# Kernel optimization log

Measured on AMD Instinct MI355X. Metric: run time of the kernel, lower is better.

Reference implementation:

```python
import jax, jax.numpy as jnp
import numpy as np

D_MODEL = 1024
D_INNER = 2048
D_STATE = 16
D_CONV = 4
DT_RANK = 64  # ceil(D_MODEL / 16)
BATCH = 2
SEQLEN = 2048


def setup_inputs() -> dict:
    key = jax.random.key(0)
    ks = jax.random.split(key, 9)
    s = 0.02
    hidden_states = jax.random.normal(ks[0], (BATCH, SEQLEN, D_MODEL), dtype=jnp.float32)
    W_in = jax.random.normal(ks[1], (D_MODEL, 2 * D_INNER), dtype=jnp.float32) * s
    # flax depthwise Conv kernel layout: (window, in_features//groups=1, out_features)
    conv_kernel = jax.random.normal(ks[2], (D_CONV, 1, D_INNER), dtype=jnp.float32) * 0.2
    conv_bias = jax.random.normal(ks[3], (D_INNER,), dtype=jnp.float32) * s
    W_x = jax.random.normal(ks[4], (D_INNER, DT_RANK + 2 * D_STATE), dtype=jnp.float32) * s
    W_dt = jax.random.normal(ks[5], (DT_RANK, D_INNER), dtype=jnp.float32) * s
    b_dt = jax.random.normal(ks[6], (D_INNER,), dtype=jnp.float32) * s
    # A_log = log(arange(1, d_state+1)) broadcast over d_inner (constant init in module)
    A_log = jnp.log(jnp.broadcast_to(jnp.arange(1, D_STATE + 1, dtype=jnp.float32), (D_INNER, D_STATE)))
    D = jnp.ones((D_INNER,), dtype=jnp.float32)
    W_out = jax.random.normal(ks[7], (D_INNER, D_MODEL), dtype=jnp.float32) * s
    return {
        "hidden_states": hidden_states,
        "W_in": W_in,
        "conv_kernel": conv_kernel,
        "conv_bias": conv_bias,
        "W_x": W_x,
        "W_dt": W_dt,
        "b_dt": b_dt,
        "A_log": A_log,
        "D": D,
        "W_out": W_out,
    }


def _mamba_forward(hidden_states, W_in, conv_kernel, conv_bias, W_x, W_dt, b_dt, A_log, D, W_out):
    # in_proj, then einops '(d i)' split with i=2 => interleaved channels
    xz = hidden_states @ W_in                       # (b, l, 2*d_inner)
    x = xz[..., 0::2]                               # (b, l, d_inner)
    z = xz[..., 1::2]                               # (b, l, d_inner)

    # depthwise conv1d, padding='SAME' (as in flax nn.Conv)
    x = jax.lax.conv_general_dilated(
        x, conv_kernel, window_strides=(1,), padding="SAME",
        dimension_numbers=("NWC", "WIO", "NWC"),
        feature_group_count=D_INNER,
    ) + conv_bias
    x = jax.nn.silu(x)

    x_dbl = x @ W_x                                 # (b, l, dt_rank + 2*d_state)
    dt = x_dbl[..., :DT_RANK] @ W_dt + b_dt         # (b, l, d_inner)
    Bm = x_dbl[..., DT_RANK:DT_RANK + D_STATE]      # (b, l, n)
    Cm = x_dbl[..., DT_RANK + D_STATE:]             # (b, l, n)

    A = -jnp.exp(A_log.astype(jnp.float32))         # (d_inner, n)
    delta = jax.nn.softplus(dt.astype(jnp.float32)) # (b, l, d_inner)

    deltaA = jnp.exp(jnp.einsum("bld,dn->lbdn", delta, A))          # (l, b, d, n)
    deltaB_u = jnp.einsum("bld,bln,bld->lbdn", delta, Bm, x)        # (l, b, d, n)
    C_l = jnp.transpose(Cm, (1, 0, 2))                               # (l, b, n)

    state0 = jnp.zeros((BATCH, D_INNER, D_STATE), dtype=jnp.float32)

    def step(state, inputs):
        dA, dBu, c = inputs
        state = dA * state + dBu                    # (b, d, n)
        y = jnp.einsum("bdn,bn->bd", state, c)      # (b, d)
        return state, y

    _, y = jax.lax.scan(step, state0, (deltaA, deltaB_u, C_l))
    y = jnp.transpose(y, (1, 0, 2))                 # (b, l, d_inner)

    out = (y + x * D) * jax.nn.silu(z)              # skip via D, gate via silu(z)
    return out @ W_out                              # (b, l, d_model)


def reference(hidden_states, W_in, conv_kernel, conv_bias, W_x, W_dt, b_dt, A_log, D, W_out):
    return _mamba_forward(hidden_states, W_in, conv_kernel, conv_bias, W_x, W_dt, b_dt, A_log, D, W_out)
```

## Files before the change

kernel.cpp:

```cpp
#include <hip/hip_runtime.h>
#include <hip/hip_bf16.h>

typedef unsigned short u16;
typedef __attribute__((ext_vector_type(8))) short short8;
typedef __attribute__((ext_vector_type(4))) short short4v;
typedef __attribute__((ext_vector_type(4))) float f32x4;
typedef __attribute__((ext_vector_type(4))) float float4v;
typedef __attribute__((ext_vector_type(2))) float f32x2;

#define DMODEL 1024
#define DI 2048
#define NST 16
#define RANK 64
#define BB 2
#define LL 2048
#define MM (BB*LL)
#define LC 32
#define NCH (LL/LC)

__device__ __forceinline__ float b2f(u16 v){ union{unsigned u; float f;}x; x.u=(unsigned)v<<16; return x.f; }
__device__ __forceinline__ u16 f2b(float f){
  union{unsigned u; float f;}x; x.f=f;
  unsigned r = x.u + 0x7FFFu + ((x.u>>16)&1u);
  return (u16)(r>>16);
}
__device__ __forceinline__ bool probe_bf(const u16* probe){ return probe[1] != 0; }
__device__ __forceinline__ float ldin(const void* p, size_t i, bool bf){
  return bf ? b2f(((const u16*)p)[i]) : ((const float*)p)[i];
}
__device__ __forceinline__ u16 ldb(const void* p, size_t i, bool bf){
  return bf ? ((const u16*)p)[i] : f2b(((const float*)p)[i]);
}
__device__ __forceinline__ void gl16(const u16* g, char* lds_wave_base){
  __builtin_amdgcn_global_load_lds((const __attribute__((address_space(1))) unsigned*)g,
                                   (__attribute__((address_space(3))) unsigned*)lds_wave_base, 16, 0, 0);
}

template<int EPI>
__global__ __launch_bounds__(256,2) void mgemm_k(
    const u16* __restrict__ A, const u16* __restrict__ Bt,
    void* __restrict__ O0, void* __restrict__ O1,
    const void* __restrict__ bias, const u16* __restrict__ probe,
    int M, int N, int K, int lda, int ldb, int ldc)
{
  const bool bf = probe_bf(probe);
  __shared__ char smem[(EPI==3||EPI==4) ? 33792 : 16384];
  const int t = threadIdx.x;
  int bx = blockIdx.x, by = blockIdx.y;
  {
    const int gx = gridDim.x;
    const int nwg = gx*gridDim.y;
    const int lin = by*gx + bx;
    const int swz = (lin & 7)*(nwg>>3) + (lin>>3);
    bx = swz % gx; by = swz / gx;
  }
  const int m0 = by*128, n0 = bx*128;
  const int kbeg = blockIdx.z * K;
  const int lane = t & 63;
  const int wv = t >> 6;
  const int wm = (wv>>1)*64, wn = (wv&1)*64;
  const int lr = lane & 15, q = lane >> 4;

  const int r0 = t>>2, q0 = t&3;
  const u16* Ag0 = A + kbeg + (size_t)(m0 + r0)*lda + q0*8;
  const u16* Ag1 = A + kbeg + (size_t)(m0 + 64 + r0)*lda + q0*8;
  const u16* Bg0 = Bt + kbeg + (size_t)(n0 + r0)*ldb + q0*8;
  const u16* Bg1 = Bt + kbeg + (size_t)(n0 + 64 + r0)*ldb + q0*8;
  char* const wbase = smem + (t & ~63)*16;
  char* const lA0 = wbase;
  char* const lA1 = wbase + 4096;
  char* const lB0 = wbase + 8192;
  char* const lB1 = wbase + 12288;

  int aro[4], bro[4];
#pragma unroll
  for(int i=0;i<4;i++) aro[i] = (wm + i*16 + lr)*64 + q*16;
#pragma unroll
  for(int j=0;j<4;j++) bro[j] = (wn + j*16 + lr)*64 + q*16;

  f32x4 acc[4][4];
#pragma unroll
  for(int i=0;i<4;i++)
#pragma unroll
    for(int j=0;j<4;j++) acc[i][j] = (f32x4){0.f,0.f,0.f,0.f};

  for(int k0=0;k0<K;k0+=32){
    __syncthreads();
    gl16(Ag0 + k0, lA0); gl16(Ag1 + k0, lA1);
    gl16(Bg0 + k0, lB0); gl16(Bg1 + k0, lB1);
    __syncthreads();
    short8 af[4], bfv[4];
#pragma unroll
    for(int i=0;i<4;i++) af[i] = *(const short8*)(smem + aro[i]);
#pragma unroll
    for(int j=0;j<4;j++) bfv[j] = *(const short8*)(smem + 8192 + bro[j]);
#pragma unroll
    for(int i=0;i<4;i++)
#pragma unroll
      for(int j=0;j<4;j++)
        acc[i][j] = __builtin_amdgcn_mfma_f32_16x16x32_bf16(af[i], bfv[j], acc[i][j], 0,0,0);
  }

  if(EPI==3 || EPI==4){
    float bj[4];
    if(EPI==3){
#pragma unroll
      for(int j=0;j<4;j++) bj[j] = ldin(bias, n0 + wn + j*16 + lr, bf);
    }
    __syncthreads();
    u16* tile = (u16*)smem;
#pragma unroll
    for(int i=0;i<4;i++)
#pragma unroll
      for(int r=0;r<4;r++){
        int trow = wm + i*16 + q*4 + r;
#pragma unroll
        for(int j=0;j<4;j++){
          int tcol = wn + j*16 + lr;
          float v = acc[i][j][r];
          if(EPI==3){
            float s = v + bj[j];
            v = (s > 20.f) ? s : log1pf(__expf(s));
          }
          tile[trow*132 + tcol] = f2b(v);
        }
      }
    __syncthreads();
    u16* obase;
    int cb;
    if(EPI==4){ obase = (n0 < DI) ? (u16*)O0 : (u16*)O1; cb = n0 & (DI-1); }
    else      { obase = (u16*)O0; cb = n0; }
    const int oc = (EPI==4) ? DI : ldc;
#pragma unroll
    for(int it=0;it<8;it++){
      int idx = it*256 + t;
      int row = idx >> 4;
      int colc = (idx & 15) * 8;
      short8 v = *(const short8*)(tile + row*132 + colc);
      *(short8*)(obase + (size_t)(m0+row)*oc + cb + colc) = v;
    }
    return;
  }
#pragma unroll
  for(int i=0;i<4;i++){
#pragma unroll
    for(int r=0;r<4;r++){
      int row = m0 + wm + i*16 + q*4 + r;
#pragma unroll
      for(int j=0;j<4;j++){
        int col = n0 + wn + j*16 + lr;
        float v = acc[i][j][r];
        if(EPI==1){
          ((float*)O0)[(size_t)blockIdx.z*M*ldc + (size_t)row*ldc + col] = v;
        } else {
          if(bf) ((u16*)O0)[(size_t)row*ldc + col] = f2b(v);
          else   ((float*)O0)[(size_t)row*ldc + col] = v;
        }
      }
    }
  }
}

__device__ __forceinline__ void tr_block(
    const void* src, u16* dst, int R, int C, int bx, int by, bool bf, bool perm,
    int tid, u16 (*tile)[33])
{
  const int c0 = bx*32, r0 = by*32;
  const int tc = tid & 31, tr0 = tid >> 5;
#pragma unroll
  for(int i=0;i<4;i++){
    int r = tr0 + i*8;
    int gc = c0 + tc;
    tile[r][tc] = (gc < C) ? ldb(src, (size_t)(r0+r)*C + gc, bf) : (u16)0;
  }
  __syncthreads();
#pragma unroll
  for(int i=0;i<4;i++){
    int dr = c0 + tr0 + i*8;
    if(perm) dr = (dr>>1) + ((dr&1)<<11);
    int dc = r0 + tc;
    dst[(size_t)dr*R + dc] = tile[tc][tr0 + i*8];
  }
}

__global__ __launch_bounds__(256) void prep_k(
    const void* __restrict__ W_in, const void* __restrict__ W_out,
    const void* __restrict__ W_x, const void* __restrict__ W_dt,
    const void* __restrict__ hidden,
    u16* __restrict__ WinT, u16* __restrict__ WoutT, u16* __restrict__ WxT,
    u16* __restrict__ WdtT, u16* __restrict__ hb, const u16* __restrict__ probe)
{
  const bool bf = probe_bf(probe);
  __shared__ u16 tile[32][33];
  const int bid = blockIdx.x, t = threadIdx.x;
  if(bid < 4096){
    tr_block(W_in, WinT, DMODEL, 2*DI, bid & 127, bid >> 7, bf, true, t, tile);
  } else if(bid < 6144){
    int b2 = bid - 4096; tr_block(W_out, WoutT, DI, DMODEL, b2 & 31, b2 >> 5, bf, false, t, tile);
  } else if(bid < 6400){
    int b2 = bid - 6144; tr_block(W_x, WxT, DI, 96, b2 & 3, b2 >> 2, bf, false, t, tile);
  } else if(bid < 6528){
    int b2 = bid - 6400; tr_block(W_dt, WdtT, RANK, DI, b2 & 63, b2 >> 6, bf, false, t, tile);
  } else {
    size_t i = ((size_t)(bid - 6528)*256 + t)*8;
    if(bf){
      *(short8*)(hb+i) = *(const short8*)((const u16*)hidden + i);
    } else {
      float4v a = *(const float4v*)((const float*)hidden + i);
      float4v b = *(const float4v*)((const float*)hidden + i + 4);
      short8 r;
      r[0]=(short)f2b(a[0]); r[1]=(short)f2b(a[1]); r[2]=(short)f2b(a[2]); r[3]=(short)f2b(a[3]);
      r[4]=(short)f2b(b[0]); r[5]=(short)f2b(b[1]); r[6]=(short)f2b(b[2]); r[7]=(short)f2b(b[3]);
      *(short8*)(hb+i) = r;
    }
  }
}

__global__ __launch_bounds__(256) void redx_k(
    const float* __restrict__ P, float* __restrict__ xdbl, u16* __restrict__ xdblb)
{
  size_t i = ((size_t)blockIdx.x*256 + threadIdx.x)*4;
  float4v s = *(const float4v*)(P + i);
#pragma unroll
  for(int p=1;p<8;p++) s += *(const float4v*)(P + (size_t)p*MM*128 + i);
  *(float4v*)(xdbl + i) = s;
  short4v r; r[0]=(short)f2b(s[0]); r[1]=(short)f2b(s[1]); r[2]=(short)f2b(s[2]); r[3]=(short)f2b(s[3]);
  *(short4v*)(xdblb + i) = r;
}

__global__ __launch_bounds__(256) void red7_k(
    const float* __restrict__ P, void* __restrict__ out, const u16* __restrict__ probe)
{
  const bool bf = probe_bf(probe);
  size_t i = ((size_t)blockIdx.x*256 + threadIdx.x)*4;
  float4v a = *(const float4v*)(P + i);
  float4v b = *(const float4v*)(P + (size_t)MM*DMODEL + i);
  float4v s = a + b;
  if(bf){
    short4v r; r[0]=(short)f2b(s[0]); r[1]=(short)f2b(s[1]); r[2]=(short)f2b(s[2]); r[3]=(short)f2b(s[3]);
    *(short4v*)((u16*)out + i) = r;
  } else {
    *(float4v*)((float*)out + i) = s;
  }
}

__global__ __launch_bounds__(256) void conv_silu_k(
  const u16* __restrict__ xb, const void* __restrict__ w,
  const void* __restrict__ bias, u16* __restrict__ xcb,
  const u16* __restrict__ probe)
{
  const bool bf = probe_bf(probe);
  const int row = blockIdx.x;
  const int tt = row & (LL-1);
  const int d = threadIdx.x*8;
  float wv[4][8], bv[8];
  if(bf){
    short8 bb = *(const short8*)((const u16*)bias + d);
#pragma unroll
    for(int j=0;j<8;j++) bv[j] = b2f((u16)bb[j]);
#pragma unroll
    for(int k=0;k<4;k++){
      short8 ww = *(const short8*)((const u16*)w + k*DI + d);
#pragma unroll
      for(int j=0;j<8;j++) wv[k][j] = b2f((u16)ww[j]);
    }
  } else {
    *(float4v*)(bv)   = *(const float4v*)((const float*)bias + d);
    *(float4v*)(bv+4) = *(const float4v*)((const float*)bias + d + 4);
#pragma unroll
    for(int k=0;k<4;k++){
      *(float4v*)(wv[k])   = *(const float4v*)((const float*)w + k*DI + d);
      *(float4v*)(wv[k]+4) = *(const float4v*)((const float*)w + k*DI + d + 4);
    }
  }
  float acc[8];
#pragma unroll
  for(int j=0;j<8;j++) acc[j] = bv[j];
  const u16* xrow = xb + (size_t)row*DI + d;
#pragma unroll
  for(int k=0;k<4;k++){
    int o = tt - 1 + k;
    if(0<=o && o<LL){
      short8 xv = *(const short8*)(xrow + (ptrdiff_t)(k-1)*DI);
#pragma unroll
      for(int j=0;j<8;j++) acc[j] = fmaf(b2f((u16)xv[j]), wv[k][j], acc[j]);
    }
  }
  short8 sb;
#pragma unroll
  for(int j=0;j<8;j++){ float s = acc[j] / (1.f + __expf(-acc[j])); sb[j]=(short)f2b(s); }
  *(short8*)(xcb + (size_t)row*DI + d) = sb;
}

__global__ __launch_bounds__(256) void scan_a_k(
  const u16* __restrict__ dlb, const u16* __restrict__ xcb,
  const float* __restrict__ xdbl, const void* __restrict__ A_log,
  float* __restrict__ Bacc, float* __restrict__ sumdv,
  const u16* __restrict__ probe)
{
  const bool bf = probe_bf(probe);
  __shared__ float Bsh[LC][NST];
  const int t = threadIdx.x;
  const int d0 = blockIdx.x*512 + 2*t;
  const int b = blockIdx.y, c = blockIdx.z;
  for(int i=t;i<LC*NST;i+=256){
    int l = i>>4, n = i&15;
    Bsh[l][n] = xdbl[((size_t)b*LL + (size_t)c*LC + l)*128 + 64 + n];
  }
  __syncthreads();
  float ac[2][NST], s[2][NST];
#pragma unroll
  for(int ch=0;ch<2;ch++)
#pragma unroll
    for(int n=0;n<NST;n++){
      ac[ch][n] = -__expf(ldin(A_log, (size_t)(d0+ch)*NST+n, bf));
      s[ch][n]=0.f;
    }
  bool geom = true;
#pragma unroll
  for(int ch=0;ch<2;ch++){
    float a0 = ac[ch][0];
#pragma unroll
    for(int n=1;n<NST;n++) geom = geom && (fabsf(ac[ch][n]-(n+1)*a0) <= 1e-4f*(n+1)*fabsf(a0));
  }
  float sum0=0.f, sum1=0.f;
  const size_t base0 = ((size_t)b*LL + (size_t)c*LC)*DI + d0;
  const u16* dptr = dlb + base0;
  const u16* xptr = xcb + base0;

  auto stepA = [&](int l, unsigned dp, unsigned xp){
    float dv0=b2f((u16)(dp&0xffff)), dv1=b2f((u16)(dp>>16));
    float xv0=b2f((u16)(xp&0xffff)), xv1=b2f((u16)(xp>>16));
    float du0=dv0*xv0, du1=dv1*xv1;
    sum0+=dv0; sum1+=dv1;
    if(geom){
      float e0=__expf(ac[0][0]*dv0), e1=__expf(ac[1][0]*dv1);
      float p0=1.f, p1=1.f;
#pragma unroll
      for(int n=0;n<NST;n++){
        float Bv=Bsh[l][n];
        p0*=e0; s[0][n]=fmaf(p0, s[0][n], du0*Bv);
        p1*=e1; s[1][n]=fmaf(p1, s[1][n], du1*Bv);
      }
    } else {
#pragma unroll
      for(int n=0;n<NST;n++){
        float Bv=Bsh[l][n];
        s[0][n]=fmaf(__expf(ac[0][n]*dv0), s[0][n], du0*Bv);
        s[1][n]=fmaf(__expf(ac[1][n]*dv1), s[1][n], du1*Bv);
      }
    }
  };

  unsigned dpA = *(const unsigned*)(dptr);
  unsigned xpA = *(const unsigned*)(xptr);
  unsigned dpB = *(const unsigned*)(dptr + DI);
  unsigned xpB = *(const unsigned*)(xptr + DI);
  for(int l=0;l<LC;l+=2){
    int l2 = (l+2 < LC) ? l+2 : LC-1;
    int l3 = (l+3 < LC) ? l+3 : LC-1;
    unsigned dpC = *(const unsigned*)(dptr + (size_t)l2*DI);
    unsigned xpC = *(const unsigned*)(xptr + (size_t)l2*DI);
    unsigned dpD = *(const unsigned*)(dptr + (size_t)l3*DI);
    unsigned xpD = *(const unsigned*)(xptr + (size_t)l3*DI);
    stepA(l,   dpA, xpA);
    stepA(l+1, dpB, xpB);
    dpA=dpC; xpA=xpC; dpB=dpD; xpB=xpD;
  }

  const size_t ob = ((size_t)c*BB + b)*((size_t)NST*DI) + d0;
#pragma unroll
  for(int n=0;n<NST;n++){
    f32x2 bs; bs[0]=s[0][n]; bs[1]=s[1][n];
    *(f32x2*)(Bacc + ob + (size_t)n*DI) = bs;
  }
  f32x2 sd; sd[0]=sum0; sd[1]=sum1;
  *(f32x2*)(sumdv + ((size_t)c*BB + b)*DI + d0) = sd;
}

__global__ __launch_bounds__(256) void scan_b_k(
  const float* __restrict__ Bacc, const float* __restrict__ sumdv,
  const void* __restrict__ A_log, float* __restrict__ Sin,
  const u16* __restrict__ probe)
{
  const bool bf = probe_bf(probe);
  const int idx = blockIdx.x*256 + threadIdx.x;
  const int d = idx & (DI-1);
  const int n = (idx >> 11) & 15;
  const int b = idx >> 15;
  const float ac = -__expf(ldin(A_log, (size_t)d*NST+n, bf));
  float s = 0.f;
  float svN = sumdv[((size_t)0*BB + b)*DI + d];
  float bbN = Bacc[idx];
  for(int c=0;c<NCH;c++){
    int c1 = (c+1 < NCH) ? c+1 : NCH-1;
    float svC = sumdv[((size_t)c1*BB + b)*DI + d];
    float bbC = Bacc[(size_t)c1*((size_t)BB*NST*DI) + idx];
    float a = __expf(ac * svN);
    Sin[(size_t)c*((size_t)BB*NST*DI) + idx] = s;
    s = fmaf(a, s, bbN);
    svN = svC; bbN = bbC;
  }
}

__global__ __launch_bounds__(256) void scan_c_gate_k(
  const u16* __restrict__ dlb, const u16* __restrict__ xcb,
  const float* __restrict__ xdbl, const void* __restrict__ A_log,
  const float* __restrict__ Sin, const u16* __restrict__ zb,
  const void* __restrict__ Dw, u16* __restrict__ G,
  const u16* __restrict__ probe)
{
  const bool bf = probe_bf(probe);
  __shared__ float Bsh[LC][NST], Csh[LC][NST];
  const int t = threadIdx.x;
  const int d0 = blockIdx.x*512 + 2*t;
  const int b = blockIdx.y, c = blockIdx.z;
  for(int i=t;i<LC*NST;i+=256){
    int l = i>>4, n = i&15;
    size_t ro = ((size_t)b*LL + (size_t)c*LC + l)*128;
    Bsh[l][n] = xdbl[ro + 64 + n];
    Csh[l][n] = xdbl[ro + 80 + n];
  }
  __syncthreads();
  float ac[2][NST], s[2][NST];
  const size_t ib = ((size_t)c*BB + b)*((size_t)NST*DI) + d0;
#pragma unroll
  for(int ch=0;ch<2;ch++)
#pragma unroll
    for(int n=0;n<NST;n++)
      ac[ch][n] = -__expf(ldin(A_log, (size_t)(d0+ch)*NST+n, bf));
#pragma unroll
  for(int n=0;n<NST;n++){
    f32x2 si = *(const f32x2*)(Sin + ib + (size_t)n*DI);
    s[0][n]=si[0]; s[1][n]=si[1];
  }
  bool geom = true;
#pragma unroll
  for(int ch=0;ch<2;ch++){
    float a0 = ac[ch][0];
#pragma unroll
    for(int n=1;n<NST;n++) geom = geom && (fabsf(ac[ch][n]-(n+1)*a0) <= 1e-4f*(n+1)*fabsf(a0));
  }
  const float D0 = ldin(Dw, d0, bf), D1 = ldin(Dw, d0+1, bf);
  const size_t base0 = ((size_t)b*LL + (size_t)c*LC)*DI + d0;
  const u16* dptr = dlb + base0;
  const u16* xptr = xcb + base0;
  const u16* zptr = zb  + base0;

  auto stepC = [&](int l, unsigned dp, unsigned xp, unsigned zz){
    float dv0=b2f((u16)(dp&0xffff)), dv1=b2f((u16)(dp>>16));
    float xv0=b2f((u16)(xp&0xffff)), xv1=b2f((u16)(xp>>16));
    float du0=dv0*xv0, du1=dv1*xv1;
    float y0=0.f, y1=0.f;
    if(geom){
      float e0=__expf(ac[0][0]*dv0), e1=__expf(ac[1][0]*dv1);
      float p0=1.f, p1=1.f;
#pragma unroll
      for(int n=0;n<NST;n++){
        float Bv=Bsh[l][n], Cv=Csh[l][n];
        p0*=e0; s[0][n]=fmaf(p0, s[0][n], du0*Bv); y0=fmaf(s[0][n], Cv, y0);
        p1*=e1; s[1][n]=fmaf(p1, s[1][n], du1*Bv); y1=fmaf(s[1][n], Cv, y1);
      }
    } else {
#pragma unroll
      for(int n=0;n<NST;n++){
        float Bv=Bsh[l][n], Cv=Csh[l][n];
        s[0][n]=fmaf(__expf(ac[0][n]*dv0), s[0][n], du0*Bv); y0=fmaf(s[0][n], Cv, y0);
        s[1][n]=fmaf(__expf(ac[1][n]*dv1), s[1][n], du1*Bv); y1=fmaf(s[1][n], Cv, y1);
      }
    }
    float z0 = b2f((u16)(zz & 0xffff)), z1 = b2f((u16)(zz >> 16));
    float g0 = z0 / (1.f + __expf(-z0));
    float g1 = z1 / (1.f + __expf(-z1));
    float o0 = (y0 + xv0*D0) * g0;
    float o1 = (y1 + xv1*D1) * g1;
    *(unsigned*)(G + base0 + (size_t)l*DI) = (unsigned)f2b(o0) | ((unsigned)f2b(o1) << 16);
  };

  unsigned dpA = *(const unsigned*)(dptr);
  unsigned xpA = *(const unsigned*)(xptr);
  unsigned zzA = *(const unsigned*)(zptr);
  unsigned dpB = *(const unsigned*)(dptr + DI);
  unsigned xpB = *(const unsigned*)(xptr + DI);
  unsigned zzB = *(const unsigned*)(zptr + DI);
  for(int l=0;l<LC;l+=2){
    int l2 = (l+2 < LC) ? l+2 : LC-1;
    int l3 = (l+3 < LC) ? l+3 : LC-1;
    unsigned dpC = *(const unsigned*)(dptr + (size_t)l2*DI);
    unsigned xpC = *(const unsigned*)(xptr + (size_t)l2*DI);
    unsigned zzC = *(const unsigned*)(zptr + (size_t)l2*DI);
    unsigned dpD = *(const unsigned*)(dptr + (size_t)l3*DI);
    unsigned xpD = *(const unsigned*)(xptr + (size_t)l3*DI);
    unsigned zzD = *(const unsigned*)(zptr + (size_t)l3*DI);
    stepC(l,   dpA, xpA, zzA);
    stepC(l+1, dpB, xpB, zzB);
    dpA=dpC; xpA=xpC; zzA=zzC; dpB=dpD; xpB=xpD; zzB=zzD;
  }
}

extern "C" void kernel_launch(void* const* d_in, const int* in_sizes, int n_in,
                              void* d_out, int out_size, void* d_ws, size_t ws_size,
                              hipStream_t stream)
{
  const void* hidden = d_in[0];
  const void* W_in   = d_in[1];
  const void* convw  = d_in[2];
  const void* convb  = d_in[3];
  const void* W_x    = d_in[4];
  const void* W_dt   = d_in[5];
  const void* b_dt   = d_in[6];
  const u16*  A_log  = (const u16*)d_in[7];
  const void* Dw     = d_in[8];
  const void* W_out  = d_in[9];

  char* p = (char*)d_ws;
  u16*   xb   = (u16*)  p;
  float* Sin  = (float*)p;
  u16*   zb   = (u16*)  (p + 16777216);
  u16*   xcb  = (u16*)  (p + 33554432);
  float* Bcc  = (float*)(p + 67108864);
  u16*   G    = (u16*)  (p + 83886080);
  float* Pw   = (float*)(p + 100663296);
  u16*   dlb  = (u16*)  (p + 100663296);
  float* Pw7  = (float*)(p + 100663296);
  u16*   hb   = (u16*)  (p + 117440512);
  float* sumdv= (float*)(p + 117440512);
  float* xdbl = (float*)(p + 134217728);
  u16*   xdblb= (u16*)  (p + 136314880);
  u16*   WinT = (u16*)  (p + 137363456);
  u16*   WoutT= (u16*)  (p + 145752064);
  u16*   WxT  = (u16*)  (p + 149946368);
  u16*   WdtT = (u16*)  (p + 150470656);

  prep_k<<<6528 + (MM*DMODEL)/(256*8), 256, 0, stream>>>(
      W_in, W_out, W_x, W_dt, hidden, WinT, WoutT, WxT, WdtT, hb, A_log);
  mgemm_k<4><<<dim3(32,32), 256, 0, stream>>>(hb, WinT, xb, zb, nullptr, A_log,
                                              MM, 2*DI, DMODEL, DMODEL, DMODEL, DI);
  conv_silu_k<<<MM, 256, 0, stream>>>(xb, convw, convb, xcb, A_log);
  mgemm_k<1><<<dim3(1,32,8), 256, 0, stream>>>(xcb, WxT, Pw, nullptr, nullptr, A_log,
                                               MM, 128, DI/8, DI, DI, 128);
  redx_k<<<(MM*128)/(256*4), 256, 0, stream>>>(Pw, xdbl, xdblb);
  mgemm_k<3><<<dim3(16,32), 256, 0, stream>>>(xdblb, WdtT, dlb, nullptr, b_dt, A_log,
                                              MM, DI, RANK, 128, RANK, DI);
  scan_a_k<<<dim3(DI/512, BB, NCH), 256, 0, stream>>>(dlb, xcb, xdbl, A_log, Bcc, sumdv, A_log);
  scan_b_k<<<(BB*NST*DI)/256, 256, 0, stream>>>(Bcc, sumdv, A_log, Sin, A_log);
  scan_c_gate_k<<<dim3(DI/512, BB, NCH), 256, 0, stream>>>(dlb, xcb, xdbl, A_log, Sin, zb, Dw, G, A_log);
  mgemm_k<1><<<dim3(DMODEL/128, MM/128, 2), 256, 0, stream>>>(G, WoutT, Pw7, nullptr, nullptr, A_log,
                                                              MM, DMODEL, DI/2, DI, DI, DMODEL);
  red7_k<<<(MM*DMODEL)/(256*4), 256, 0, stream>>>(Pw7, d_out, A_log);
}
```

Measured before the change: 321.6 us.

## Add 256x256 double-buffered LDS GEMM for in_proj and out_proj

Adds a new 512-thread GEMM kernel with 256x256 output tiles, a K step of 64, an XOR-swizzled LDS layout, and double-buffered global-to-LDS loads. It waits on vmcnt, raises wave priority with setprio around the MFMA groups, and interleaves fragment loads with compute. The in_proj and out_proj GEMMs switch to this kernel, and out_proj now uses split-K of 4 with the partial buffer moved, so the reduction kernel sums four partials. The aim is more data reuse per tile and better overlap of loads with MFMA. In exchange it uses 128KB of LDS per block, so occupancy drops, and out_proj writes and reads twice as many fp32 partials.

```diff
diff --git a/kernel.cpp b/kernel.cpp
--- a/kernel.cpp
+++ b/kernel.cpp
@@ -37,6 +37,167 @@
 }
 
 template<int EPI>
+__global__ __launch_bounds__(512,2) void mgemm256_k(
+    const u16* __restrict__ A, const u16* __restrict__ Bt,
+    void* __restrict__ O0, void* __restrict__ O1,
+    int M, int N, int K, int lda, int ldb, int ldc)
+{
+  __shared__ char smem[131072];
+  const int t = threadIdx.x;
+  int bx = blockIdx.x, by = blockIdx.y;
+  {
+    const int gx = gridDim.x;
+    const int nwg = gx*gridDim.y;
+    const int lin = by*gx + bx;
+    const int swz = (lin & 7)*(nwg>>3) + (lin>>3);
+    bx = swz % gx; by = swz / gx;
+  }
+  const int m0 = by*256, n0 = bx*256;
+  const int kbeg = blockIdx.z * K;
+  const int wv = t >> 6, ln = t & 63;
+  const int wr = wv >> 2, wc = wv & 3;
+  const int lr = ln & 15, q = ln >> 4;
+  const int NT = K >> 6;
+
+  const int srow = ln >> 3;
+  const int koff = ((ln & 7) ^ srow) * 8;
+  const u16* AgP[4]; const u16* BgP[4];
+#pragma unroll
+  for(int c=0;c<4;c++){
+    AgP[c] = A + (size_t)(m0 + (c*8+wv)*8 + srow)*lda + kbeg + koff;
+    BgP[c] = Bt + (size_t)(n0 + (c*8+wv)*8 + srow)*ldb + kbeg + koff;
+  }
+
+  const int ck = ((q ^ (ln & 7)) * 16);
+  int aro[8], bro[4];
+#pragma unroll
+  for(int i=0;i<8;i++) aro[i] = (wr*128 + i*16 + lr)*128 + ck;
+#pragma unroll
+  for(int j=0;j<4;j++) bro[j] = (wc*64 + j*16 + lr)*128 + ck;
+
+  f32x4 acc[8][4];
+#pragma unroll
+  for(int i=0;i<8;i++)
+#pragma unroll
+    for(int j=0;j<4;j++) acc[i][j] = (f32x4){0.f,0.f,0.f,0.f};
+
+  auto stage = [&](int kt, int cur){
+    char* ab = smem + cur*65536;
+    char* bb = ab + 32768;
+#pragma unroll
+    for(int c=0;c<4;c++) gl16(AgP[c] + kt*64, ab + (c*8+wv)*1024);
+#pragma unroll
+    for(int c=0;c<4;c++) gl16(BgP[c] + kt*64, bb + (c*8+wv)*1024);
+  };
+
+  stage(0,0);
+  stage(1,1);
+
+  for(int kt=0; kt<NT; ++kt){
+    const int cur = kt & 1;
+    if(kt == NT-1) asm volatile("s_waitcnt vmcnt(0)" ::: "memory");
+    else           asm volatile("s_waitcnt vmcnt(8)" ::: "memory");
+    __builtin_amdgcn_sched_barrier(0);
+    __builtin_amdgcn_s_barrier();
+    __builtin_amdgcn_sched_barrier(0);
+    const char* ab = smem + cur*65536;
+    const char* bb = ab + 32768;
+    short8 afr[4], bfr[4];
+#pragma unroll
+    for(int j=0;j<4;j++) bfr[j] = *(const short8*)(bb + bro[j]);
+#pragma unroll
+    for(int i=0;i<4;i++) afr[i] = *(const short8*)(ab + aro[i]);
+    __builtin_amdgcn_s_setprio(1);
+#pragma unroll
+    for(int i=0;i<4;i++)
+#pragma unroll
+      for(int j=0;j<4;j++)
+        acc[i][j] = __builtin_amdgcn_mfma_f32_16x16x32_bf16(afr[i], bfr[j], acc[i][j], 0,0,0);
+    __builtin_amdgcn_s_setprio(0);
+#pragma unroll
+    for(int i=0;i<4;i++) afr[i] = *(const short8*)(ab + aro[4+i]);
+    __builtin_amdgcn_s_setprio(1);
+#pragma unroll
+    for(int i=0;i<4;i++)
+#pragma unroll
+      for(int j=0;j<4;j++)
+        acc[4+i][j] = __builtin_amdgcn_mfma_f32_16x16x32_bf16(afr[i], bfr[j], acc[4+i][j], 0,0,0);
+    __builtin_amdgcn_s_setprio(0);
+#pragma unroll
+    for(int j=0;j<4;j++) bfr[j] = *(const short8*)(bb + (bro[j]^64));
+#pragma unroll
+    for(int i=0;i<4;i++) afr[i] = *(const short8*)(ab + (aro[i]^64));
+    __builtin_amdgcn_s_setprio(1);
+#pragma unroll
+    for(int i=0;i<4;i++)
+#pragma unroll
+      for(int j=0;j<4;j++)
+        acc[i][j] = __builtin_amdgcn_mfma_f32_16x16x32_bf16(afr[i], bfr[j], acc[i][j], 0,0,0);
+    __builtin_amdgcn_s_setprio(0);
+#pragma unroll
+    for(int i=0;i<4;i++) afr[i] = *(const short8*)(ab + (aro[4+i]^64));
+    asm volatile("s_waitcnt lgkmcnt(0)" ::: "memory");
+    __builtin_amdgcn_sched_barrier(0);
+    __builtin_amdgcn_s_barrier();
+    __builtin_amdgcn_sched_barrier(0);
+    if(kt+2 < NT) stage(kt+2, cur);
+    __builtin_amdgcn_sched_barrier(0);
+    __builtin_amdgcn_s_setprio(1);
+#pragma unroll
+    for(int i=0;i<4;i++)
+#pragma unroll
+      for(int j=0;j<4;j++)
+        acc[4+i][j] = __builtin_amdgcn_mfma_f32_16x16x32_bf16(afr[i], bfr[j], acc[4+i][j], 0,0,0);
+    __builtin_amdgcn_s_setprio(0);
+  }
+
+  if(EPI==4){
+    u16* tile = (u16*)smem;
+    u16* obase = (n0 < DI) ? (u16*)O0 : (u16*)O1;
+    const int cb = n0 & (DI-1);
+    for(int h=0;h<2;h++){
+      __builtin_amdgcn_s_barrier();
+      if(wr == h){
+#pragma unroll
+        for(int i=0;i<8;i++)
+#pragma unroll
+          for(int r=0;r<4;r++){
+            int trow = i*16 + q*4 + r;
+#pragma unroll
+            for(int j=0;j<4;j++)
+              tile[trow*264 + wc*64 + j*16 + lr] = f2b(acc[i][j][r]);
+          }
+      }
+      asm volatile("s_waitcnt lgkmcnt(0)" ::: "memory");
+      __builtin_amdgcn_sched_barrier(0);
+      __builtin_amdgcn_s_barrier();
+      __builtin_amdgcn_sched_barrier(0);
+#pragma unroll
+      for(int it=0;it<8;it++){
+        int idx = it*512 + t;
+        int row = idx >> 5;
+        int ch  = (idx & 31) * 8;
+        short8 v = *(const short8*)(tile + row*264 + ch);
+        *(short8*)(obase + (size_t)(m0 + h*128 + row)*ldc + cb + ch) = v;
+      }
+    }
+    return;
+  }
+#pragma unroll
+  for(int i=0;i<8;i++){
+#pragma unroll
+    for(int r=0;r<4;r++){
+      int row = m0 + wr*128 + i*16 + q*4 + r;
+#pragma unroll
+      for(int j=0;j<4;j++){
+        int col = n0 + wc*64 + j*16 + lr;
+        ((float*)O0)[(size_t)blockIdx.z*M*ldc + (size_t)row*ldc + col] = acc[i][j][r];
+      }
+    }
+  }
+}
+
+template<int EPI>
 __global__ __launch_bounds__(256,2) void mgemm_k(
     const u16* __restrict__ A, const u16* __restrict__ Bt,
     void* __restrict__ O0, void* __restrict__ O1,
@@ -44,7 +205,7 @@
     int M, int N, int K, int lda, int ldb, int ldc)
 {
   const bool bf = probe_bf(probe);
-  __shared__ char smem[(EPI==3||EPI==4) ? 33792 : 16384];
+  __shared__ char smem[(EPI==3) ? 33792 : 16384];
   const int t = threadIdx.x;
   int bx = blockIdx.x, by = blockIdx.y;
   {
@@ -101,12 +262,10 @@
         acc[i][j] = __builtin_amdgcn_mfma_f32_16x16x32_bf16(af[i], bfv[j], acc[i][j], 0,0,0);
   }
 
-  if(EPI==3 || EPI==4){
+  if(EPI==3){
     float bj[4];
-    if(EPI==3){
-#pragma unroll
-      for(int j=0;j<4;j++) bj[j] = ldin(bias, n0 + wn + j*16 + lr, bf);
-    }
+#pragma unroll
+    for(int j=0;j<4;j++) bj[j] = ldin(bias, n0 + wn + j*16 + lr, bf);
     __syncthreads();
     u16* tile = (u16*)smem;
 #pragma unroll
@@ -117,27 +276,19 @@
 #pragma unroll
         for(int j=0;j<4;j++){
           int tcol = wn + j*16 + lr;
-          float v = acc[i][j][r];
-          if(EPI==3){
-            float s = v + bj[j];
-            v = (s > 20.f) ? s : log1pf(__expf(s));
-          }
-          tile[trow*132 + tcol] = f2b(v);
+          float s = acc[i][j][r] + bj[j];
+          float sp = (s > 20.f) ? s : log1pf(__expf(s));
+          tile[trow*132 + tcol] = f2b(sp);
         }
       }
     __syncthreads();
-    u16* obase;
-    int cb;
-    if(EPI==4){ obase = (n0 < DI) ? (u16*)O0 : (u16*)O1; cb = n0 & (DI-1); }
-    else      { obase = (u16*)O0; cb = n0; }
-    const int oc = (EPI==4) ? DI : ldc;
 #pragma unroll
     for(int it=0;it<8;it++){
       int idx = it*256 + t;
       int row = idx >> 4;
       int colc = (idx & 15) * 8;
       short8 v = *(const short8*)(tile + row*132 + colc);
-      *(short8*)(obase + (size_t)(m0+row)*oc + cb + colc) = v;
+      *(short8*)((u16*)O0 + (size_t)(m0+row)*ldc + n0 + colc) = v;
     }
     return;
   }
@@ -149,13 +300,7 @@
 #pragma unroll
       for(int j=0;j<4;j++){
         int col = n0 + wn + j*16 + lr;
-        float v = acc[i][j][r];
-        if(EPI==1){
-          ((float*)O0)[(size_t)blockIdx.z*M*ldc + (size_t)row*ldc + col] = v;
-        } else {
-          if(bf) ((u16*)O0)[(size_t)row*ldc + col] = f2b(v);
-          else   ((float*)O0)[(size_t)row*ldc + col] = v;
-        }
+        ((float*)O0)[(size_t)blockIdx.z*M*ldc + (size_t)row*ldc + col] = acc[i][j][r];
       }
     }
   }
@@ -233,9 +378,9 @@
 {
   const bool bf = probe_bf(probe);
   size_t i = ((size_t)blockIdx.x*256 + threadIdx.x)*4;
-  float4v a = *(const float4v*)(P + i);
-  float4v b = *(const float4v*)(P + (size_t)MM*DMODEL + i);
-  float4v s = a + b;
+  float4v s = *(const float4v*)(P + i);
+#pragma unroll
+  for(int p=1;p<4;p++) s += *(const float4v*)(P + (size_t)p*MM*DMODEL + i);
   if(bf){
     short4v r; r[0]=(short)f2b(s[0]); r[1]=(short)f2b(s[1]); r[2]=(short)f2b(s[2]); r[3]=(short)f2b(s[3]);
     *(short4v*)((u16*)out + i) = r;
@@ -516,13 +661,13 @@
   char* p = (char*)d_ws;
   u16*   xb   = (u16*)  p;
   float* Sin  = (float*)p;
+  float* Pw7  = (float*)p;
   u16*   zb   = (u16*)  (p + 16777216);
   u16*   xcb  = (u16*)  (p + 33554432);
   float* Bcc  = (float*)(p + 67108864);
   u16*   G    = (u16*)  (p + 83886080);
   float* Pw   = (float*)(p + 100663296);
   u16*   dlb  = (u16*)  (p + 100663296);
-  float* Pw7  = (float*)(p + 100663296);
   u16*   hb   = (u16*)  (p + 117440512);
   float* sumdv= (float*)(p + 117440512);
   float* xdbl = (float*)(p + 134217728);
@@ -534,8 +679,8 @@
 
   prep_k<<<6528 + (MM*DMODEL)/(256*8), 256, 0, stream>>>(
       W_in, W_out, W_x, W_dt, hidden, WinT, WoutT, WxT, WdtT, hb, A_log);
-  mgemm_k<4><<<dim3(32,32), 256, 0, stream>>>(hb, WinT, xb, zb, nullptr, A_log,
-                                              MM, 2*DI, DMODEL, DMODEL, DMODEL, DI);
+  mgemm256_k<4><<<dim3(16,16), 512, 0, stream>>>(hb, WinT, xb, zb,
+                                                 MM, 2*DI, DMODEL, DMODEL, DMODEL, DI);
   conv_silu_k<<<MM, 256, 0, stream>>>(xb, convw, convb, xcb, A_log);
   mgemm_k<1><<<dim3(1,32,8), 256, 0, stream>>>(xcb, WxT, Pw, nullptr, nullptr, A_log,
                                                MM, 128, DI/8, DI, DI, 128);
@@ -545,7 +690,7 @@
   scan_a_k<<<dim3(DI/512, BB, NCH), 256, 0, stream>>>(dlb, xcb, xdbl, A_log, Bcc, sumdv, A_log);
   scan_b_k<<<(BB*NST*DI)/256, 256, 0, stream>>>(Bcc, sumdv, A_log, Sin, A_log);
   scan_c_gate_k<<<dim3(DI/512, BB, NCH), 256, 0, stream>>>(dlb, xcb, xdbl, A_log, Sin, zb, Dw, G, A_log);
-  mgemm_k<1><<<dim3(DMODEL/128, MM/128, 2), 256, 0, stream>>>(G, WoutT, Pw7, nullptr, nullptr, A_log,
-                                                              MM, DMODEL, DI/2, DI, DI, DMODEL);
+  mgemm256_k<1><<<dim3(4,16,4), 512, 0, stream>>>(G, WoutT, Pw7, nullptr,
+                                                  MM, DMODEL, DI/4, DI, DI, DMODEL);
   red7_k<<<(MM*DMODEL)/(256*4), 256, 0, stream>>>(Pw7, d_out, A_log);
 }
```

After: 325.3 us. Within noise of the previous version (+1.1%).
